# Kernel optimization log

Hardware: AMD Instinct MI355X
Metric: run time of the kernel (lower is better)

The kernel has to match this reference:

```python
import jax, jax.numpy as jnp
import numpy as np

BS, N, C = 512, 18, 2048
EPS = 1e-12
BN_SCALE = 1.0 / np.sqrt(1.0 + 1e-5)  # eval-mode BN with running_mean=0, running_var=1


def _normalize(v):
    # F.normalize(p=2, dim=2, eps=1e-12)
    n = jnp.linalg.norm(v, axis=2, keepdims=True)
    return v / jnp.maximum(n, EPS)


def _bn_relu(v, gamma, beta):
    # BatchNorm2d in eval mode (running_mean=0, running_var=1) followed by ReLU
    return jax.nn.relu(v * (gamma * BN_SCALE) + beta)


def _safe_sqrt(r):
    # forward-identical to sqrt (r >= 0 here); avoids NaN grad at r == 0 (diagonal)
    pos = r > 0
    return jnp.where(pos, jnp.sqrt(jnp.where(pos, r, 1.0)), 0.0)


def setup_inputs() -> dict:
    key = jax.random.key(0)
    ks = jax.random.split(key, 10)
    s = 0.02
    return {
        "x": jax.random.normal(ks[0], (BS, N, C), jnp.float32),
        "part_coordinate": jax.random.uniform(ks[1], (BS, N, 4), jnp.float32),
        # conv1: C -> 3 (1x1)
        "w1": jax.random.normal(ks[2], (3, C), jnp.float32) * s,
        "b1": jnp.zeros((3,), jnp.float32),
        # conv2: 4 -> C, BN, ReLU, C -> 3
        "w2a": jax.random.normal(ks[3], (C, 4), jnp.float32) * s,
        "b2a": jnp.zeros((C,), jnp.float32),
        "g2": jnp.ones((C,), jnp.float32),
        "be2": jnp.zeros((C,), jnp.float32),
        "w2b": jax.random.normal(ks[4], (3, C), jnp.float32) * s,
        "b2b": jnp.zeros((3,), jnp.float32),
        # conv: C -> C, BN, ReLU
        "wc": jax.random.normal(ks[5], (C, C), jnp.float32) * s,
        "bc": jnp.zeros((C,), jnp.float32),
        "gc": jnp.ones((C,), jnp.float32),
        "bec": jnp.zeros((C,), jnp.float32),
        # conv3: C -> C, BN, ReLU
        "w3": jax.random.normal(ks[6], (C, C), jnp.float32) * s,
        "b3": jnp.zeros((C,), jnp.float32),
        "g3": jnp.ones((C,), jnp.float32),
        "be3": jnp.zeros((C,), jnp.float32),
    }


def reference(x, part_coordinate, w1, b1, w2a, b2a, g2, be2, w2b, b2b,
              wc, bc, gc, bec, w3, b3, g3, be3):
    # z1 = softmax(conv1(x)) over the 3 clusters
    z1 = jax.nn.softmax(jnp.einsum('bnc,kc->bnk', x, w1) + b1, axis=2)  # [B,N,3]

    # distance_list1: cosine affinities of x and z1
    xn = _normalize(x)
    d1_1 = jnp.einsum('bnc,bmc->bnm', xn, xn)       # [B,N,N]
    z1n = _normalize(z1)
    d2_1 = jnp.einsum('bnk,bmk->bnm', z1n, z1n)     # [B,N,N]

    # z2 = softmax(conv2(part_coordinate))
    h = _bn_relu(jnp.einsum('bnf,cf->bnc', part_coordinate, w2a) + b2a, g2, be2)
    z2 = jax.nn.softmax(jnp.einsum('bnc,kc->bnk', h, w2b) + b2b, axis=2)  # [B,N,3]

    # distance_list2: spatial-center distance + cosine affinity of z2
    yc = part_coordinate[..., 0] + jnp.floor(part_coordinate[..., 2] / 2)
    xc = part_coordinate[..., 1] + jnp.floor(part_coordinate[..., 3] / 2)
    dy = (yc[:, None, :] - yc[:, :, None]) ** 2
    dx = (xc[:, None, :] - xc[:, :, None]) ** 2
    d1_2 = 1.0 - 2.0 * _safe_sqrt(dx + dy)          # [B,N,N]
    z2n = _normalize(z2)
    d2_2 = jnp.einsum('bnk,bmk->bnm', z2n, z2n)     # [B,N,N]

    # encode / decode aggregation over 3 cluster nodes
    z = z1 + z2                                      # [B,N,3]
    enc = z / (jnp.sum(z, axis=1, keepdims=True) + EPS)
    dec = z / (jnp.sum(z, axis=2, keepdims=True) + EPS)
    u = jnp.einsum('bnk,bnc->bkc', enc, x)           # [B,3,C]
    u = _bn_relu(jnp.einsum('bkc,dc->bkd', u, wc) + bc, gc, bec)
    y = jnp.einsum('bnk,bkc->bnc', dec, u)           # [B,N,C]
    y = _bn_relu(jnp.einsum('bnc,dc->bnd', y, w3) + b3, g3, be3) + x

    return (y, d2_1, d1_1, d2_2, d1_2)
```

## Files before the change

### kernel.cpp

```cpp
#include <hip/hip_runtime.h>

#define BS   512
#define NPTS 18
#define CH   2048
#define EPSF 1e-12f
#define BNS  0.9999950000374997f

typedef unsigned short ushort_t;
typedef __attribute__((ext_vector_type(8)))  short bfrag;
typedef __attribute__((ext_vector_type(4)))  float f32x4v;
typedef __attribute__((ext_vector_type(16))) float f32x16;

__device__ inline ushort_t bf16_rne(float f) {
  union { float f; unsigned int u; } c; c.f = f;
  unsigned int u = c.u;
  u += 0x7fffu + ((u >> 16) & 1u);
  return (ushort_t)(u >> 16);
}
__device__ inline float bf16_to_f(ushort_t s) {
  union { float f; unsigned int u; } c; c.u = ((unsigned int)s) << 16;
  return c.f;
}
__device__ inline bfrag cvt8(float4 a, float4 b) {
  bfrag r;
  r[0]=(short)bf16_rne(a.x); r[1]=(short)bf16_rne(a.y);
  r[2]=(short)bf16_rne(a.z); r[3]=(short)bf16_rne(a.w);
  r[4]=(short)bf16_rne(b.x); r[5]=(short)bf16_rne(b.y);
  r[6]=(short)bf16_rne(b.z); r[7]=(short)bf16_rne(b.w);
  return r;
}

__global__ __launch_bounds__(1024, 8) void k_mega(
    const float* __restrict__ x, const float* __restrict__ pc,
    const float* __restrict__ w1, const float* __restrict__ b1,
    const float* __restrict__ w2a, const float* __restrict__ b2a,
    const float* __restrict__ g2, const float* __restrict__ be2,
    const float* __restrict__ w2b, const float* __restrict__ b2b,
    const float* __restrict__ wc, const float* __restrict__ w3,
    ushort_t* __restrict__ wc_bf, ushort_t* __restrict__ w3_bf,
    float* __restrict__ d21, float* __restrict__ d11,
    float* __restrict__ d22, float* __restrict__ d12,
    ushort_t* __restrict__ u_pre, float* __restrict__ dec_out)
{
  const int blk = blockIdx.x, tid = threadIdx.x;

  if (blk >= BS) {
    const int cb = blk - BS;
    const int n4 = CH*CH/4;
    #pragma unroll
    for (int k = 0; k < 4; k++) {
      int gid = cb*4096 + k*1024 + tid;
      const float* src; ushort_t* dst; int i;
      if (gid < n4) { src = wc; dst = wc_bf; i = gid; }
      else          { src = w3; dst = w3_bf; i = gid - n4; }
      float4 v = ((const float4*)src)[i];
      ushort4 o;
      o.x = bf16_rne(v.x); o.y = bf16_rne(v.y);
      o.z = bf16_rne(v.z); o.w = bf16_rne(v.w);
      ((ushort4*)dst)[i] = o;
    }
    return;
  }

  __shared__ __align__(16) ushort_t IMG[18*CH];
  __shared__ __align__(16) float F[2048];
  float* Gt     = F;
  float* l2part = F + 1512;
  float* l2s    = F + 1620;
  float* z1s    = F + 1674;
  float* z2s    = F + 1728;
  float* encs   = F + 1782;
  float* ycs    = F + 1836;
  float* xcs    = F + 1854;
  float* n1inv  = F + 1872;
  float* n2inv  = F + 1890;
  float* rinvS  = F + 1908;
  float* colinv = F + 1926;

  const int b = blk, lane = tid & 63, wv = tid >> 6;

  {
    const float4* x4 = (const float4*)x + (size_t)b*9216;
    #pragma unroll
    for (int k = 0; k < 4; k++) {
      int p = k*1024 + tid;
      float4 a = x4[2*p], c = x4[2*p + 1];
      int row = p >> 8;
      *(bfrag*)((char*)IMG + ((p*16) ^ ((row & 7) << 4))) = cvt8(a, c);
    }
    if (tid < 512) {
      int p = 4096 + tid;
      float4 a = x4[2*p], c = x4[2*p + 1];
      int row = p >> 8;
      *(bfrag*)((char*)IMG + ((p*16) ^ ((row & 7) << 4))) = cvt8(a, c);
    }
  }
  __syncthreads();

  if (wv < 4) {
    const int rc = lane & 31, kh = lane >> 5;
    const int arow = (rc < NPTS) ? rc : (NPTS-1);
    const int amsk = (arow & 7) << 4;
    const int abase = arow*4096;
    const bool isw = (rc >= NPTS) && (rc < NPTS+3);
    const int wrow = isw ? (rc - NPTS) : 0;
    const float* wp = w1 + (size_t)wrow*CH + wv*512 + kh*8;
    f32x16 acc = {0.f,0.f,0.f,0.f,0.f,0.f,0.f,0.f,0.f,0.f,0.f,0.f,0.f,0.f,0.f,0.f};
    #pragma unroll 4
    for (int j = 0; j < 32; j++) {
      const int kb = (wv*512 + j*16 + kh*8)*2;
      bfrag av = *(const bfrag*)((const char*)IMG + ((abase + kb) ^ amsk));
      bfrag bv = av;
      if (isw) bv = cvt8(*(const float4*)(wp + j*16), *(const float4*)(wp + j*16 + 4));
      acc = __builtin_amdgcn_mfma_f32_32x32x16_bf16(av, bv, acc, 0, 0, 0);
    }
    #pragma unroll
    for (int r = 0; r < 16; r++) {
      int orow = (r & 3) + 8*(r >> 2) + 4*kh;
      if (orow < NPTS && rc < 21) Gt[wv*378 + orow*21 + rc] = acc[r];
    }
  } else {
    const int zid = wv - 4, g = zid >> 1, th = zid & 1;
    const float* pcb = pc + (size_t)b*NPTS*4 + g*12;
    float pq[3][4];
    #pragma unroll
    for (int j = 0; j < 3; j++) {
      pq[j][0] = pcb[j*4+0]; pq[j][1] = pcb[j*4+1];
      pq[j][2] = pcb[j*4+2]; pq[j][3] = pcb[j*4+3];
    }
    float acc[3][3];
    #pragma unroll
    for (int j = 0; j < 3; j++) { acc[j][0]=0.f; acc[j][1]=0.f; acc[j][2]=0.f; }
    #pragma unroll 2
    for (int it = 0; it < 16; it++) {
      int c = th*1024 + it*64 + lane;
      const float4 wa = *(const float4*)(w2a + (size_t)c*4);
      float bb = b2a[c], gg = g2[c]*BNS, be = be2[c];
      float wb0 = w2b[c], wb1 = w2b[CH+c], wb2 = w2b[2*CH+c];
      #pragma unroll
      for (int j = 0; j < 3; j++) {
        float v = fmaf(pq[j][3], wa.w, fmaf(pq[j][2], wa.z,
                  fmaf(pq[j][1], wa.y, fmaf(pq[j][0], wa.x, bb))));
        float h = fmaxf(fmaf(v, gg, be), 0.f);
        acc[j][0] = fmaf(h, wb0, acc[j][0]);
        acc[j][1] = fmaf(h, wb1, acc[j][1]);
        acc[j][2] = fmaf(h, wb2, acc[j][2]);
      }
    }
    #pragma unroll
    for (int j = 0; j < 3; j++)
      #pragma unroll
      for (int k = 0; k < 3; k++) {
        float v = acc[j][k];
        #pragma unroll
        for (int off = 32; off; off >>= 1) v += __shfl_xor(v, off);
        if (lane == 0) l2part[zid*9 + j*3 + k] = v;
      }
  }
  __syncthreads();

  if (tid < 378) {
    F[tid] = (F[tid] + F[378+tid]) + (F[756+tid] + F[1134+tid]);
  } else if (tid < 432) {
    int t = tid - 378;
    int p = t/3, k = t - 3*p, g = p/3, pp = p - 3*g;
    l2s[t] = l2part[(g*2)*9 + pp*3+k] + l2part[(g*2+1)*9 + pp*3+k] + b2b[k];
  } else if (tid >= 448 && tid < 466) {
    int n = tid - 448;
    const float* p = pc + (size_t)b*NPTS*4 + n*4;
    ycs[n] = p[0] + floorf(p[2]*0.5f);
    xcs[n] = p[1] + floorf(p[3]*0.5f);
  }
  __syncthreads();
  float* sGl = F;

  if (tid < NPTS) {
    int n = tid;
    float a0 = sGl[n*21+18] + b1[0], a1 = sGl[n*21+19] + b1[1], a2 = sGl[n*21+20] + b1[2];
    float mx = fmaxf(a0, fmaxf(a1, a2));
    float e0 = expf(a0-mx), e1 = expf(a1-mx), e2 = expf(a2-mx);
    float inv = 1.f/(e0+e1+e2);
    float z10 = e0*inv, z11 = e1*inv, z12 = e2*inv;
    z1s[n*3+0]=z10; z1s[n*3+1]=z11; z1s[n*3+2]=z12;
    n1inv[n] = 1.f/fmaxf(sqrtf(z10*z10+z11*z11+z12*z12), EPSF);

    float c0 = l2s[n*3+0], c1 = l2s[n*3+1], c2 = l2s[n*3+2];
    mx = fmaxf(c0, fmaxf(c1, c2));
    e0 = expf(c0-mx); e1 = expf(c1-mx); e2 = expf(c2-mx);
    inv = 1.f/(e0+e1+e2);
    float z20 = e0*inv, z21 = e1*inv, z22 = e2*inv;
    z2s[n*3+0]=z20; z2s[n*3+1]=z21; z2s[n*3+2]=z22;
    n2inv[n] = 1.f/fmaxf(sqrtf(z20*z20+z21*z21+z22*z22), EPSF);

    float zr0 = z10+z20, zr1 = z11+z21, zr2 = z12+z22;
    float rinvv = 1.f/((zr0+zr1+zr2) + EPSF);
    dec_out[(size_t)b*54 + n*3 + 0] = zr0*rinvv;
    dec_out[(size_t)b*54 + n*3 + 1] = zr1*rinvv;
    dec_out[(size_t)b*54 + n*3 + 2] = zr2*rinvv;

    rinvS[n] = 1.f/fmaxf(sqrtf(sGl[n*21+n]), EPSF);
  }
  __syncthreads();

  if (tid < 3) {
    float s = 0.f;
    #pragma unroll
    for (int n = 0; n < NPTS; n++) s += z1s[n*3+tid] + z2s[n*3+tid];
    colinv[tid] = 1.f/(s + EPSF);
  }
  if (tid < NPTS*NPTS) {
    int t = tid;
    int n = t/NPTS, mm = t - n*NPTS;
    float dd21 = (z1s[n*3]*z1s[mm*3] + z1s[n*3+1]*z1s[mm*3+1] + z1s[n*3+2]*z1s[mm*3+2])
                 * n1inv[n]*n1inv[mm];
    float dd22 = (z2s[n*3]*z2s[mm*3] + z2s[n*3+1]*z2s[mm*3+1] + z2s[n*3+2]*z2s[mm*3+2])
                 * n2inv[n]*n2inv[mm];
    float dd11 = sGl[n*21+mm] * rinvS[n]*rinvS[mm];
    float dyv = ycs[mm]-ycs[n], dxv = xcs[mm]-xcs[n];
    float r = dxv*dxv + dyv*dyv;
    float dd12 = 1.f - 2.f*((r > 0.f) ? sqrtf(r) : 0.f);
    size_t o = (size_t)b*NPTS*NPTS + t;
    d21[o] = dd21; d11[o] = dd11; d22[o] = dd22; d12[o] = dd12;
  }
  __syncthreads();
  if (tid < 54) encs[tid] = (z1s[tid]+z2s[tid])*colinv[tid%3];
  __syncthreads();

  {
    const int c0 = tid*2;
    float a0=0.f,a1=0.f,a2=0.f, q0=0.f,q1=0.f,q2=0.f;
    #pragma unroll
    for (int n = 0; n < NPTS; n++) {
      unsigned v = *(const unsigned*)((const char*)IMG + ((n*4096 + c0*2) ^ ((n & 7) << 4)));
      float x0 = bf16_to_f((ushort_t)(v & 0xffff));
      float x1 = bf16_to_f((ushort_t)(v >> 16));
      float e0 = encs[n*3+0], e1 = encs[n*3+1], e2 = encs[n*3+2];
      a0 = fmaf(e0, x0, a0); q0 = fmaf(e0, x1, q0);
      a1 = fmaf(e1, x0, a1); q1 = fmaf(e1, x1, q1);
      a2 = fmaf(e2, x0, a2); q2 = fmaf(e2, x1, q2);
    }
    ushort2 o0, o1, o2;
    o0.x = bf16_rne(a0); o0.y = bf16_rne(q0);
    o1.x = bf16_rne(a1); o1.y = bf16_rne(q1);
    o2.x = bf16_rne(a2); o2.y = bf16_rne(q2);
    *(ushort2*)(u_pre + ((size_t)b*3 + 0)*CH + c0) = o0;
    *(ushort2*)(u_pre + ((size_t)b*3 + 1)*CH + c0) = o1;
    *(ushort2*)(u_pre + ((size_t)b*3 + 2)*CH + c0) = o2;
  }
}

#define GM 1536
#define GK 2048
#define GN 2048

#define STAGE(buf, k0) { \
    _Pragma("unroll") \
    for (int i = 0; i < 4; i++) \
      __builtin_amdgcn_global_load_lds( \
          (const __attribute__((address_space(1))) void*)(Ag + (size_t)(i*32 + ldrow)*GK + (k0)), \
          (__attribute__((address_space(3))) void*)(&Asm[buf][i*2048 + wv*512]), 16, 0, 0); \
    _Pragma("unroll") \
    for (int i = 0; i < 2; i++) \
      __builtin_amdgcn_global_load_lds( \
          (const __attribute__((address_space(1))) void*)(Bg + (size_t)(i*32 + ldrow)*GK + (k0)), \
          (__attribute__((address_space(3))) void*)(&Bsm[buf][i*2048 + wv*512]), 16, 0, 0); }

__global__ __launch_bounds__(256) void gemm1(
    const ushort_t* __restrict__ A, const ushort_t* __restrict__ B,
    ushort_t* __restrict__ Cout, const float* __restrict__ bias,
    const float* __restrict__ gamma, const float* __restrict__ beta)
{
  __shared__ ushort_t Asm[2][128*64];
  __shared__ ushort_t Bsm[2][64*64];
  const int tid  = threadIdx.x;
  const int lane = tid & 63, wv = tid >> 6;
  const int mb = blockIdx.x % (GM/128), nb = blockIdx.x / (GM/128);
  const int wr = (wv >> 1) * 64, wc = (wv & 1) * 32;

  f32x4v acc[4][2];
  #pragma unroll
  for (int m = 0; m < 4; m++)
    #pragma unroll
    for (int n = 0; n < 2; n++)
      acc[m][n] = (f32x4v){0.f, 0.f, 0.f, 0.f};

  const int ldrow = tid >> 3;
  const int ldcol = (((tid & 7) ^ (ldrow & 7)) * 8);
  const ushort_t* Ag = A + (size_t)(mb*128)*GK + ldcol;
  const ushort_t* Bg = B + (size_t)(nb*64)*GK + ldcol;
  const int r15 = lane & 15, khi = lane >> 4;

  STAGE(0, 0)
  __syncthreads();
  for (int t = 0; t < GK/64; ++t) {
    const int cur = t & 1;
    if (t < GK/64 - 1) STAGE(cur ^ 1, (t+1)*64)
    #pragma unroll
    for (int ks = 0; ks < 2; ks++) {
      bfrag af[4], bfv[2];
      #pragma unroll
      for (int m = 0; m < 4; m++) {
        const int ar = wr + m*16 + r15;
        af[m] = *(const bfrag*)(&Asm[cur][ar*64 + ((ks*32 + khi*8) ^ ((ar & 7)*8))]);
      }
      #pragma unroll
      for (int n = 0; n < 2; n++) {
        const int br = wc + n*16 + r15;
        bfv[n] = *(const bfrag*)(&Bsm[cur][br*64 + ((ks*32 + khi*8) ^ ((br & 7)*8))]);
      }
      #pragma unroll
      for (int m = 0; m < 4; m++)
        #pragma unroll
        for (int n = 0; n < 2; n++)
          acc[m][n] = __builtin_amdgcn_mfma_f32_16x16x32_bf16(
              af[m], bfv[n], acc[m][n], 0, 0, 0);
    }
    __syncthreads();
  }

  #pragma unroll
  for (int n = 0; n < 2; n++) {
    const int gc = nb*64 + wc + n*16 + r15;
    float bi = bias[gc], ga = gamma[gc]*BNS, be = beta[gc];
    #pragma unroll
    for (int m = 0; m < 4; m++) {
      const int gr0 = mb*128 + wr + m*16 + khi*4;
      #pragma unroll
      for (int r = 0; r < 4; r++) {
        float v = fmaxf(fmaf(acc[m][n][r] + bi, ga, be), 0.f);
        Cout[(size_t)(gr0 + r)*GN + gc] = bf16_rne(v);
      }
    }
  }
}

#define STAGE2(buf, k0) { \
    _Pragma("unroll") \
    for (int i = 0; i < 3; i++) { \
      int u = i*256 + tid; \
      int arw = u >> 3, ac8 = u & 7; \
      __builtin_amdgcn_global_load_lds( \
          (const __attribute__((address_space(1))) void*)(Au + (size_t)(mb*96 + arw)*GK + (k0) + ((ac8 ^ (arw & 7))*8)), \
          (__attribute__((address_space(3))) void*)(&A2[buf][u*8]), 16, 0, 0); \
    } \
    _Pragma("unroll") \
    for (int i = 0; i < 2; i++) { \
      int u = i*256 + tid; \
      int brw = u >> 3, bc8 = u & 7; \
      __builtin_amdgcn_global_load_lds( \
          (const __attribute__((address_space(1))) void*)(Bw + (size_t)(nb*64 + brw)*GK + (k0) + ((bc8 ^ (brw & 7))*8)), \
          (__attribute__((address_space(3))) void*)(&B2[buf][u*8]), 16, 0, 0); \
    } }

__global__ __launch_bounds__(256) void gemm_epi(
    const ushort_t* __restrict__ Au, const ushort_t* __restrict__ Bw,
    const float* __restrict__ x, const float* __restrict__ dec,
    const float* __restrict__ b3, const float* __restrict__ g3,
    const float* __restrict__ be3, float* __restrict__ y)
{
  __shared__ ushort_t A2[2][96*64];
  __shared__ ushort_t B2[2][64*64];
  __shared__ ushort_t Vl[96*68];
  __shared__ float decl[32*54];
  __shared__ float mul_[64], add_[64];
  const int tid = threadIdx.x, lane = tid & 63, wv = tid >> 6;
  const int wg = (blockIdx.x & 7)*64 + (blockIdx.x >> 3);
  const int mb = wg & 15, nb = wg >> 4;
  const int wr = (wv >> 1)*48, wc = (wv & 1)*32;
  const int r15 = lane & 15, khi = lane >> 4;

  for (int i = tid; i < 32*54; i += 256) decl[i] = dec[(size_t)mb*1728 + i];
  if (tid < 64) {
    float mu = g3[nb*64 + tid]*BNS;
    mul_[tid] = mu;
    add_[tid] = fmaf(b3[nb*64 + tid], mu, be3[nb*64 + tid]);
  }

  f32x4v acc[3][2];
  #pragma unroll
  for (int m = 0; m < 3; m++)
    #pragma unroll
    for (int n = 0; n < 2; n++)
      acc[m][n] = (f32x4v){0.f, 0.f, 0.f, 0.f};

  STAGE2(0, 0)
  __syncthreads();
  for (int t = 0; t < GK/64; ++t) {
    const int cur = t & 1;
    if (t < GK/64 - 1) STAGE2(cur ^ 1, (t+1)*64)
    #pragma unroll
    for (int ks = 0; ks < 2; ks++) {
      bfrag af[3], bfv[2];
      #pragma unroll
      for (int m = 0; m < 3; m++) {
        const int ar = wr + m*16 + r15;
        af[m] = *(const bfrag*)(&A2[cur][ar*64 + ((ks*32 + khi*8) ^ ((ar & 7)*8))]);
      }
      #pragma unroll
      for (int n = 0; n < 2; n++) {
        const int br = wc + n*16 + r15;
        bfv[n] = *(const bfrag*)(&B2[cur][br*64 + ((ks*32 + khi*8) ^ ((br & 7)*8))]);
      }
      #pragma unroll
      for (int m = 0; m < 3; m++)
        #pragma unroll
        for (int n = 0; n < 2; n++)
          acc[m][n] = __builtin_amdgcn_mfma_f32_16x16x32_bf16(
              af[m], bfv[n], acc[m][n], 0, 0, 0);
    }
    __syncthreads();
  }

  #pragma unroll
  for (int n = 0; n < 2; n++) {
    const int gcl = wc + n*16 + r15;
    #pragma unroll
    for (int m = 0; m < 3; m++) {
      const int gr0 = wr + m*16 + khi*4;
      #pragma unroll
      for (int r = 0; r < 4; r++)
        Vl[(gr0 + r)*68 + gcl] = bf16_rne(acc[m][n][r]);
    }
  }
  __syncthreads();

  {
    const int bb = tid >> 3, cg = tid & 7;
    float vr[3][8], mu[8], ad[8];
    #pragma unroll
    for (int k = 0; k < 3; k++) {
      ushort4 v0 = *(const ushort4*)(&Vl[(bb*3 + k)*68 + cg*8]);
      ushort4 v1 = *(const ushort4*)(&Vl[(bb*3 + k)*68 + cg*8 + 4]);
      vr[k][0]=bf16_to_f(v0.x); vr[k][1]=bf16_to_f(v0.y);
      vr[k][2]=bf16_to_f(v0.z); vr[k][3]=bf16_to_f(v0.w);
      vr[k][4]=bf16_to_f(v1.x); vr[k][5]=bf16_to_f(v1.y);
      vr[k][6]=bf16_to_f(v1.z); vr[k][7]=bf16_to_f(v1.w);
    }
    #pragma unroll
    for (int j = 0; j < 8; j++) { mu[j] = mul_[cg*8+j]; ad[j] = add_[cg*8+j]; }

    const size_t rowbase = ((size_t)(mb*32 + bb)*NPTS)*CH + nb*64 + cg*8;
    for (int n = 0; n < NPTS; n++) {
      float d0 = decl[bb*54 + n*3 + 0];
      float d1 = decl[bb*54 + n*3 + 1];
      float d2 = decl[bb*54 + n*3 + 2];
      const float* xr = x + rowbase + (size_t)n*CH;
      float* yr = y + rowbase + (size_t)n*CH;
      #pragma unroll
      for (int cc = 0; cc < 2; cc++) {
        float4 xv = *(const float4*)(xr + cc*4);
        float4 o;
        #pragma unroll
        for (int j = 0; j < 4; j++) {
          int c = cc*4 + j;
          float val = fmaf(d0, vr[0][c], fmaf(d1, vr[1][c], d2*vr[2][c]));
          float res = fmaxf(fmaf(val, mu[c], ad[c]), 0.f);
          ((float*)&o)[j] = res + ((const float*)&xv)[j];
        }
        *(float4*)(yr + cc*4) = o;
      }
    }
  }
}

extern "C" void kernel_launch(void* const* d_in, const int* in_sizes, int n_in,
                              void* d_out, int out_size, void* d_ws, size_t ws_size,
                              hipStream_t stream) {
  const float* x   = (const float*)d_in[0];
  const float* pc  = (const float*)d_in[1];
  const float* w1  = (const float*)d_in[2];
  const float* b1  = (const float*)d_in[3];
  const float* w2a = (const float*)d_in[4];
  const float* b2a = (const float*)d_in[5];
  const float* g2  = (const float*)d_in[6];
  const float* be2 = (const float*)d_in[7];
  const float* w2b = (const float*)d_in[8];
  const float* b2b = (const float*)d_in[9];
  const float* wc  = (const float*)d_in[10];
  const float* bc  = (const float*)d_in[11];
  const float* gc  = (const float*)d_in[12];
  const float* bec = (const float*)d_in[13];
  const float* w3  = (const float*)d_in[14];
  const float* b3  = (const float*)d_in[15];
  const float* g3  = (const float*)d_in[16];
  const float* be3 = (const float*)d_in[17];

  float* out = (float*)d_out;
  float* y   = out;
  float* d21 = out + (size_t)BS*NPTS*CH;
  float* d11 = d21 + (size_t)BS*NPTS*NPTS;
  float* d22 = d11 + (size_t)BS*NPTS*NPTS;
  float* d12 = d22 + (size_t)BS*NPTS*NPTS;

  char* ybytes = (char*)y;
  ushort_t* u_pre_bf = (ushort_t*)(ybytes + 0);
  ushort_t* wc_bf    = (ushort_t*)(ybytes + 6291456);

  ushort_t* u_bf  = (ushort_t*)d_ws;
  ushort_t* w3_bf = (ushort_t*)((char*)d_ws + 6291456);
  float*    decb  = (float*)((char*)d_ws + 14680064);

  k_mega<<<BS + 512, 1024, 0, stream>>>(x, pc, w1, b1, w2a, b2a, g2, be2,
                                        w2b, b2b, wc, w3, wc_bf, w3_bf,
                                        d21, d11, d22, d12, u_pre_bf, decb);
  gemm1<<<(GM/128)*(GN/64), 256, 0, stream>>>(u_pre_bf, wc_bf, u_bf, bc, gc, bec);
  gemm_epi<<<512, 256, 0, stream>>>(u_bf, w3_bf, x, decb, b3, g3, be3, y);
}
```

Baseline: 131.7 us.

## Halve k_mega block size and redistribute per-thread work across fewer waves

```diff
diff --git a/kernel.cpp b/kernel.cpp
--- a/kernel.cpp
+++ b/kernel.cpp
@@ -30,7 +30,7 @@
   return r;
 }
 
-__global__ __launch_bounds__(1024, 8) void k_mega(
+__global__ __launch_bounds__(512, 4) void k_mega(
     const float* __restrict__ x, const float* __restrict__ pc,
     const float* __restrict__ w1, const float* __restrict__ b1,
     const float* __restrict__ w2a, const float* __restrict__ b2a,
@@ -48,8 +48,8 @@
     const int cb = blk - BS;
     const int n4 = CH*CH/4;
     #pragma unroll
-    for (int k = 0; k < 4; k++) {
-      int gid = cb*4096 + k*1024 + tid;
+    for (int k = 0; k < 8; k++) {
+      int gid = (cb*8 + k)*512 + tid;
       const float* src; ushort_t* dst; int i;
       if (gid < n4) { src = wc; dst = wc_bf; i = gid; }
       else          { src = w3; dst = w3_bf; i = gid - n4; }
@@ -66,30 +66,24 @@
   __shared__ __align__(16) float F[2048];
   float* Gt     = F;
   float* l2part = F + 1512;
-  float* l2s    = F + 1620;
-  float* z1s    = F + 1674;
-  float* z2s    = F + 1728;
-  float* encs   = F + 1782;
-  float* ycs    = F + 1836;
-  float* xcs    = F + 1854;
-  float* n1inv  = F + 1872;
-  float* n2inv  = F + 1890;
-  float* rinvS  = F + 1908;
-  float* colinv = F + 1926;
+  float* l2s    = F + 1572;
+  float* z1s    = F + 1626;
+  float* z2s    = F + 1680;
+  float* encs   = F + 1734;
+  float* ycs    = F + 1788;
+  float* xcs    = F + 1806;
+  float* n1inv  = F + 1824;
+  float* n2inv  = F + 1842;
+  float* rinvS  = F + 1860;
+  float* colinv = F + 1878;
 
   const int b = blk, lane = tid & 63, wv = tid >> 6;
 
   {
     const float4* x4 = (const float4*)x + (size_t)b*9216;
     #pragma unroll
-    for (int k = 0; k < 4; k++) {
-      int p = k*1024 + tid;
-      float4 a = x4[2*p], c = x4[2*p + 1];
-      int row = p >> 8;
-      *(bfrag*)((char*)IMG + ((p*16) ^ ((row & 7) << 4))) = cvt8(a, c);
-    }
-    if (tid < 512) {
-      int p = 4096 + tid;
+    for (int k = 0; k < 9; k++) {
+      int p = k*512 + tid;
       float4 a = x4[2*p], c = x4[2*p + 1];
       int row = p >> 8;
       *(bfrag*)((char*)IMG + ((p*16) ^ ((row & 7) << 4))) = cvt8(a, c);
@@ -120,25 +114,28 @@
       if (orow < NPTS && rc < 21) Gt[wv*378 + orow*21 + rc] = acc[r];
     }
   } else {
-    const int zid = wv - 4, g = zid >> 1, th = zid & 1;
-    const float* pcb = pc + (size_t)b*NPTS*4 + g*12;
-    float pq[3][4];
-    #pragma unroll
-    for (int j = 0; j < 3; j++) {
-      pq[j][0] = pcb[j*4+0]; pq[j][1] = pcb[j*4+1];
-      pq[j][2] = pcb[j*4+2]; pq[j][3] = pcb[j*4+3];
-    }
-    float acc[3][3];
-    #pragma unroll
-    for (int j = 0; j < 3; j++) { acc[j][0]=0.f; acc[j][1]=0.f; acc[j][2]=0.f; }
+    const int zid = wv - 4;
+    const int p0 = zid*5;
+    const int np = (zid == 3) ? 3 : 5;
+    const float* pcb = pc + (size_t)b*NPTS*4 + p0*4;
+    float pq[5][4];
+    #pragma unroll
+    for (int j = 0; j < 5; j++) {
+      int jj = (j < np) ? j : 0;
+      pq[j][0] = pcb[jj*4+0]; pq[j][1] = pcb[jj*4+1];
+      pq[j][2] = pcb[jj*4+2]; pq[j][3] = pcb[jj*4+3];
+    }
+    float acc[5][3];
+    #pragma unroll
+    for (int j = 0; j < 5; j++) { acc[j][0]=0.f; acc[j][1]=0.f; acc[j][2]=0.f; }
     #pragma unroll 2
-    for (int it = 0; it < 16; it++) {
-      int c = th*1024 + it*64 + lane;
+    for (int it = 0; it < 32; it++) {
+      int c = it*64 + lane;
       const float4 wa = *(const float4*)(w2a + (size_t)c*4);
       float bb = b2a[c], gg = g2[c]*BNS, be = be2[c];
       float wb0 = w2b[c], wb1 = w2b[CH+c], wb2 = w2b[2*CH+c];
       #pragma unroll
-      for (int j = 0; j < 3; j++) {
+      for (int j = 0; j < 5; j++) {
         float v = fmaf(pq[j][3], wa.w, fmaf(pq[j][2], wa.z,
                   fmaf(pq[j][1], wa.y, fmaf(pq[j][0], wa.x, bb))));
         float h = fmaxf(fmaf(v, gg, be), 0.f);
@@ -148,14 +145,17 @@
       }
     }
     #pragma unroll
-    for (int j = 0; j < 3; j++)
-      #pragma unroll
-      for (int k = 0; k < 3; k++) {
-        float v = acc[j][k];
+    for (int j = 0; j < 5; j++) {
+      if (j < np) {
         #pragma unroll
-        for (int off = 32; off; off >>= 1) v += __shfl_xor(v, off);
-        if (lane == 0) l2part[zid*9 + j*3 + k] = v;
-      }
+        for (int k = 0; k < 3; k++) {
+          float v = acc[j][k];
+          #pragma unroll
+          for (int off = 32; off; off >>= 1) v += __shfl_xor(v, off);
+          if (lane == 0) l2part[zid*15 + j*3 + k] = v;
+        }
+      }
+    }
   }
   __syncthreads();
 
@@ -163,8 +163,8 @@
     F[tid] = (F[tid] + F[378+tid]) + (F[756+tid] + F[1134+tid]);
   } else if (tid < 432) {
     int t = tid - 378;
-    int p = t/3, k = t - 3*p, g = p/3, pp = p - 3*g;
-    l2s[t] = l2part[(g*2)*9 + pp*3+k] + l2part[(g*2+1)*9 + pp*3+k] + b2b[k];
+    int p = t/3, k = t - 3*p, zid = p/5, pp = p - 5*zid;
+    l2s[t] = l2part[zid*15 + pp*3 + k] + b2b[k];
   } else if (tid >= 448 && tid < 466) {
     int n = tid - 448;
     const float* p = pc + (size_t)b*NPTS*4 + n*4;
@@ -227,25 +227,30 @@
   __syncthreads();
 
   {
-    const int c0 = tid*2;
-    float a0=0.f,a1=0.f,a2=0.f, q0=0.f,q1=0.f,q2=0.f;
-    #pragma unroll
+    const int c0 = tid*4;
+    float av0[4], av1[4], av2[4];
+    #pragma unroll
+    for (int j = 0; j < 4; j++) { av0[j]=0.f; av1[j]=0.f; av2[j]=0.f; }
+    #pragma unroll 2
     for (int n = 0; n < NPTS; n++) {
-      unsigned v = *(const unsigned*)((const char*)IMG + ((n*4096 + c0*2) ^ ((n & 7) << 4)));
-      float x0 = bf16_to_f((ushort_t)(v & 0xffff));
-      float x1 = bf16_to_f((ushort_t)(v >> 16));
+      ushort4 xv = *(const ushort4*)((const char*)IMG + ((n*4096 + c0*2) ^ ((n & 7) << 4)));
       float e0 = encs[n*3+0], e1 = encs[n*3+1], e2 = encs[n*3+2];
-      a0 = fmaf(e0, x0, a0); q0 = fmaf(e0, x1, q0);
-      a1 = fmaf(e1, x0, a1); q1 = fmaf(e1, x1, q1);
-      a2 = fmaf(e2, x0, a2); q2 = fmaf(e2, x1, q2);
-    }
-    ushort2 o0, o1, o2;
-    o0.x = bf16_rne(a0); o0.y = bf16_rne(q0);
-    o1.x = bf16_rne(a1); o1.y = bf16_rne(q1);
-    o2.x = bf16_rne(a2); o2.y = bf16_rne(q2);
-    *(ushort2*)(u_pre + ((size_t)b*3 + 0)*CH + c0) = o0;
-    *(ushort2*)(u_pre + ((size_t)b*3 + 1)*CH + c0) = o1;
-    *(ushort2*)(u_pre + ((size_t)b*3 + 2)*CH + c0) = o2;
+      float x0 = bf16_to_f(xv.x), x1 = bf16_to_f(xv.y);
+      float x2 = bf16_to_f(xv.z), x3 = bf16_to_f(xv.w);
+      av0[0]=fmaf(e0,x0,av0[0]); av0[1]=fmaf(e0,x1,av0[1]);
+      av0[2]=fmaf(e0,x2,av0[2]); av0[3]=fmaf(e0,x3,av0[3]);
+      av1[0]=fmaf(e1,x0,av1[0]); av1[1]=fmaf(e1,x1,av1[1]);
+      av1[2]=fmaf(e1,x2,av1[2]); av1[3]=fmaf(e1,x3,av1[3]);
+      av2[0]=fmaf(e2,x0,av2[0]); av2[1]=fmaf(e2,x1,av2[1]);
+      av2[2]=fmaf(e2,x2,av2[2]); av2[3]=fmaf(e2,x3,av2[3]);
+    }
+    ushort4 o0, o1, o2;
+    o0.x=bf16_rne(av0[0]); o0.y=bf16_rne(av0[1]); o0.z=bf16_rne(av0[2]); o0.w=bf16_rne(av0[3]);
+    o1.x=bf16_rne(av1[0]); o1.y=bf16_rne(av1[1]); o1.z=bf16_rne(av1[2]); o1.w=bf16_rne(av1[3]);
+    o2.x=bf16_rne(av2[0]); o2.y=bf16_rne(av2[1]); o2.z=bf16_rne(av2[2]); o2.w=bf16_rne(av2[3]);
+    *(ushort4*)(u_pre + ((size_t)b*3 + 0)*CH + c0) = o0;
+    *(ushort4*)(u_pre + ((size_t)b*3 + 1)*CH + c0) = o1;
+    *(ushort4*)(u_pre + ((size_t)b*3 + 2)*CH + c0) = o2;
   }
 }
 
@@ -500,9 +505,9 @@
   ushort_t* w3_bf = (ushort_t*)((char*)d_ws + 6291456);
   float*    decb  = (float*)((char*)d_ws + 14680064);
 
-  k_mega<<<BS + 512, 1024, 0, stream>>>(x, pc, w1, b1, w2a, b2a, g2, be2,
-                                        w2b, b2b, wc, w3, wc_bf, w3_bf,
-                                        d21, d11, d22, d12, u_pre_bf, decb);
+  k_mega<<<BS + 512, 512, 0, stream>>>(x, pc, w1, b1, w2a, b2a, g2, be2,
+                                       w2b, b2b, wc, w3, wc_bf, w3_bf,
+                                       d21, d11, d22, d12, u_pre_bf, decb);
   gemm1<<<(GM/128)*(GN/64), 256, 0, stream>>>(u_pre_bf, wc_bf, u_bf, bc, gc, bec);
   gemm_epi<<<512, 256, 0, stream>>>(u_bf, w3_bf, x, decb, b3, g3, be3, y);
 }
```

After: 127.5 us (median of 3 runs). 1.03x faster.
